# Kernel tuning notes

Measured on AMD Instinct MI355X. Metric: run time of the kernel, lower is better.

Reference implementation:

```python
import jax, jax.numpy as jnp
import numpy as np

H = 16      # num_head
D = 1024    # feat_dim
DK = D // H # per-head dim
B, S = 2, 2048


def setup_inputs() -> dict:
    key = jax.random.key(0)
    ks = jax.random.split(key, 11)
    scale = 1.0 / np.sqrt(D)
    inp = {
        'query': jax.random.normal(ks[0], (B, S, D), jnp.float32),
        'key':   jax.random.normal(ks[1], (B, S, D), jnp.float32),
        'value': jax.random.normal(ks[2], (B, S, D), jnp.float32),
        # causal lower-triangular mask (seq, seq); 0 entries get -1e9
        'mask':  jnp.tril(jnp.ones((S, S), jnp.int32)),
        # torch nn.Linear params: y = x @ W.T + b
        'w_q': jax.random.normal(ks[3], (D, D), jnp.float32) * scale,
        'b_q': jax.random.normal(ks[4], (D,), jnp.float32) * scale,
        'w_k': jax.random.normal(ks[5], (D, D), jnp.float32) * scale,
        'b_k': jax.random.normal(ks[6], (D,), jnp.float32) * scale,
        'w_v': jax.random.normal(ks[7], (D, D), jnp.float32) * scale,
        'b_v': jax.random.normal(ks[8], (D,), jnp.float32) * scale,
        'w_out': jax.random.normal(ks[9], (D, D), jnp.float32) * scale,
        'b_out': jax.random.normal(ks[10], (D,), jnp.float32) * scale,
    }
    return inp


def reference(query, key, value, mask, w_q, b_q, w_k, b_k, w_v, b_v, w_out, b_out):
    b = query.shape[0]
    # projections + split heads -> (b, h, s, d_k)
    def proj(x, w, bias):
        y = x @ w.T + bias
        return y.reshape(b, -1, H, DK).transpose(0, 2, 1, 3)
    q = proj(query, w_q, b_q)
    k = proj(key, w_k, b_k)
    v = proj(value, w_v, b_v)
    # scaled dot-product attention with materialized score matrix
    scores = jnp.einsum('bhqd,bhkd->bhqk', q, k) / np.sqrt(DK).astype(jnp.float32)
    scores = jnp.where(mask == 0, jnp.float32(-1e9), scores)
    attn = jax.nn.softmax(scores, axis=-1)  # dropout is identity in eval mode
    x = jnp.einsum('bhqk,bhkd->bhqd', attn, v)
    x = x.transpose(0, 2, 1, 3).reshape(b, -1, H * DK)
    return x @ w_out.T + b_out
```

## Files before the change

### kernel.cpp

```cpp
#include <hip/hip_runtime.h>

typedef unsigned short u16;
typedef __attribute__((ext_vector_type(8))) short short8;
typedef __attribute__((ext_vector_type(8))) unsigned short u16x8;
typedef __attribute__((ext_vector_type(4))) float floatx4;

#define S2LOG 0.18033688f

__device__ __forceinline__ u16 f2bf(float f) {
    unsigned int u = __float_as_uint(f);
    return (u16)((u + 0x7FFFu + ((u >> 16) & 1u)) >> 16);
}
__device__ __forceinline__ u16 f2bf_hu(float f) {
    return (u16)((__float_as_uint(f) + 0x8000u) >> 16);
}
__device__ __forceinline__ void gl_lds16(const u16* g, u16* l) {
    __builtin_amdgcn_global_load_lds(
        (const __attribute__((address_space(1))) void*)g,
        (__attribute__((address_space(3))) void*)l, 16, 0, 0);
}

__global__ __launch_bounds__(256) void cvt_all(
    const float* __restrict__ q, const float* __restrict__ k, const float* __restrict__ v,
    const float* __restrict__ wq, const float* __restrict__ wk,
    const float* __restrict__ wv, const float* __restrict__ wo,
    u16* __restrict__ ws)
{
    const int b = blockIdx.x, t = threadIdx.x;
    const float* src; u16* dst; long blk;
    if      (b < 2048) { src = q;  dst = ws;            blk = b; }
    else if (b < 4096) { src = k;  dst = ws + 4194304;  blk = b - 2048; }
    else if (b < 6144) { src = v;  dst = ws + 8388608;  blk = b - 4096; }
    else if (b < 6656) { src = wq; dst = ws + 12582912; blk = b - 6144; }
    else if (b < 7168) { src = wk; dst = ws + 13631488; blk = b - 6656; }
    else if (b < 7680) { src = wv; dst = ws + 14680064; blk = b - 7168; }
    else               { src = wo; dst = ws + 15728640; blk = b - 7680; }
    const long i = blk * 2048 + (long)t * 8;
    const float4 a = *(const float4*)(src + i);
    const float4 c = *(const float4*)(src + i + 4);
    u16x8 o;
    o[0] = f2bf(a.x); o[1] = f2bf(a.y); o[2] = f2bf(a.z); o[3] = f2bf(a.w);
    o[4] = f2bf(c.x); o[5] = f2bf(c.y); o[6] = f2bf(c.z); o[7] = f2bf(c.w);
    *(u16x8*)(dst + i) = o;
}

__device__ __forceinline__ void gemm_core64(
    const u16* __restrict__ A, const u16* __restrict__ Bw,
    int m0, int n0, floatx4 (&acc)[2][4])
{
    __shared__ u16 As[2][128 * 64];
    __shared__ u16 Bs[2][64 * 64];
    const int t = threadIdx.x, w = t >> 6;
    const int lane = t & 63, col = lane & 15, quad = lane >> 4;
    const int c7 = col & 7;

#pragma unroll
    for (int i = 0; i < 2; ++i)
#pragma unroll
        for (int j = 0; j < 4; ++j) acc[i][j] = (floatx4)0.f;

    auto stage = [&](int k0, int buf) {
#pragma unroll
        for (int jj = 0; jj < 4; ++jj) {
            const int c = jj * 256 + t;
            const int row = c >> 3, kc = (c & 7) ^ (row & 7);
            gl_lds16(A + (size_t)(m0 + row) * 1024 + k0 + kc * 8,
                     As[buf] + (jj * 256 + w * 64) * 8);
        }
#pragma unroll
        for (int jj = 0; jj < 2; ++jj) {
            const int c = jj * 256 + t;
            const int row = c >> 3, kc = (c & 7) ^ (row & 7);
            gl_lds16(Bw + (size_t)(n0 + row) * 1024 + k0 + kc * 8,
                     Bs[buf] + (jj * 256 + w * 64) * 8);
        }
    };

    stage(0, 0);
    int cur = 0;
    for (int k0 = 0; k0 < 1024; k0 += 64) {
        asm volatile("s_waitcnt vmcnt(0)" ::: "memory");
        __builtin_amdgcn_s_barrier();
        if (k0 + 64 < 1024) stage(k0 + 64, cur ^ 1);
#pragma unroll
        for (int ks = 0; ks < 2; ++ks) {
            const int swz = (ks * 4 + quad) ^ c7;
            short8 af[2], bf[4];
#pragma unroll
            for (int i = 0; i < 2; ++i)
                af[i] = *(const short8*)&As[cur][((w * 32 + i * 16 + col) * 8 + swz) * 8];
#pragma unroll
            for (int j = 0; j < 4; ++j)
                bf[j] = *(const short8*)&Bs[cur][((j * 16 + col) * 8 + swz) * 8];
#pragma unroll
            for (int i = 0; i < 2; ++i)
#pragma unroll
                for (int j = 0; j < 4; ++j)
                    acc[i][j] = __builtin_amdgcn_mfma_f32_16x16x32_bf16(
                        af[i], bf[j], acc[i][j], 0, 0, 0);
        }
        asm volatile("s_waitcnt lgkmcnt(0)" ::: "memory");
        cur ^= 1;
    }
}

__device__ __forceinline__ void gemm_core128(
    const u16* __restrict__ A, const u16* __restrict__ Bw,
    int m0, int n0, floatx4 (&acc)[4][4])
{
    __shared__ u16 As[2][128 * 32];
    __shared__ u16 Bs[2][128 * 32];
    const int t = threadIdx.x, w = t >> 6;
    const int lane = t & 63, col = lane & 15, quad = lane >> 4;
    const int wr = (w >> 1) * 64, wc = (w & 1) * 64;
    const int swz = quad ^ (col & 3) ^ ((col >> 2) & 3);

#pragma unroll
    for (int i = 0; i < 4; ++i)
#pragma unroll
        for (int j = 0; j < 4; ++j) acc[i][j] = (floatx4)0.f;

    auto stage = [&](int k0, int buf) {
#pragma unroll
        for (int jj = 0; jj < 2; ++jj) {
            const int c = jj * 256 + t;
            const int row = c >> 2;
            const int kc = (c & 3) ^ (row & 3) ^ ((row >> 2) & 3);
            gl_lds16(A + (size_t)(m0 + row) * 1024 + k0 + kc * 8,
                     As[buf] + (jj * 256 + w * 64) * 8);
            gl_lds16(Bw + (size_t)(n0 + row) * 1024 + k0 + kc * 8,
                     Bs[buf] + (jj * 256 + w * 64) * 8);
        }
    };

    stage(0, 0);
    int cur = 0;
    for (int k0 = 0; k0 < 1024; k0 += 32) {
        asm volatile("s_waitcnt vmcnt(0)" ::: "memory");
        __builtin_amdgcn_s_barrier();
        if (k0 + 32 < 1024) stage(k0 + 32, cur ^ 1);
        short8 af[4], bf[4];
#pragma unroll
        for (int i = 0; i < 4; ++i)
            af[i] = *(const short8*)&As[cur][((wr + i * 16 + col) * 4 + swz) * 8];
#pragma unroll
        for (int j = 0; j < 4; ++j)
            bf[j] = *(const short8*)&Bs[cur][((wc + j * 16 + col) * 4 + swz) * 8];
        __builtin_amdgcn_s_setprio(1);
#pragma unroll
        for (int i = 0; i < 4; ++i)
#pragma unroll
            for (int j = 0; j < 4; ++j)
                acc[i][j] = __builtin_amdgcn_mfma_f32_16x16x32_bf16(
                    af[i], bf[j], acc[i][j], 0, 0, 0);
        __builtin_amdgcn_s_setprio(0);
        asm volatile("s_waitcnt lgkmcnt(0)" ::: "memory");
        cur ^= 1;
    }
}

__global__ __launch_bounds__(256) void gemm_qkv(
    const u16* __restrict__ xq, const u16* __restrict__ xk, const u16* __restrict__ xv,
    const u16* __restrict__ wqb, const u16* __restrict__ wkb, const u16* __restrict__ wvb,
    const float* __restrict__ bq, const float* __restrict__ bk, const float* __restrict__ bv,
    u16* __restrict__ Qh, u16* __restrict__ Kh, u16* __restrict__ Vt)
{
    const int z = blockIdx.z;
    const u16*   A    = z == 0 ? xq  : z == 1 ? xk  : xv;
    const u16*   Bw   = z == 0 ? wqb : z == 1 ? wkb : wvb;
    const float* bias = z == 0 ? bq  : z == 1 ? bk  : bv;
    u16*         out  = z == 0 ? Qh  : z == 1 ? Kh  : Vt;
    const float  scale = z == 0 ? S2LOG : 1.0f;
    const int m0 = blockIdx.x * 128, n0 = blockIdx.y * 128;

    floatx4 acc[4][4];
    gemm_core128(A, Bw, m0, n0, acc);

    const int t = threadIdx.x, w = t >> 6;
    const int lane = t & 63, col = lane & 15, quad = lane >> 4;
    const int wr = (w >> 1) * 64, wc = (w & 1) * 64;
#pragma unroll
    for (int i = 0; i < 4; ++i)
#pragma unroll
        for (int j = 0; j < 4; ++j)
#pragma unroll
            for (int reg = 0; reg < 4; ++reg) {
                const int gm = m0 + wr + i * 16 + quad * 4 + reg;
                const int gn = n0 + wc + j * 16 + col;
                const float val = (acc[i][j][reg] + bias[gn]) * scale;
                const int bb = gm >> 11, ss = gm & 2047, hh = gn >> 6, dd = gn & 63;
                if (z != 2)
                    out[(((size_t)bb * 16 + hh) * 2048 + ss) * 64 + dd] = f2bf(val);
                else
                    out[(((size_t)bb * 16 + hh) * 64 + dd) * 2048 + ss] = f2bf(val);
            }
}

__global__ __launch_bounds__(256) void gemm_out(
    const u16* __restrict__ A, const u16* __restrict__ Bw,
    const float* __restrict__ bias, float* __restrict__ out)
{
    const int m0 = blockIdx.x * 128, n0 = blockIdx.y * 64;
    floatx4 acc[2][4];
    gemm_core64(A, Bw, m0, n0, acc);
    const int t = threadIdx.x, w = t >> 6;
    const int lane = t & 63, col = lane & 15, quad = lane >> 4;
#pragma unroll
    for (int i = 0; i < 2; ++i)
#pragma unroll
        for (int j = 0; j < 4; ++j)
#pragma unroll
            for (int reg = 0; reg < 4; ++reg) {
                const int gm = m0 + w * 32 + i * 16 + quad * 4 + reg;
                const int gn = n0 + j * 16 + col;
                out[(size_t)gm * 1024 + gn] = acc[i][j][reg] + bias[gn];
            }
}

__global__ __launch_bounds__(256) void attn_mfma(
    const u16* __restrict__ Qh, const u16* __restrict__ Kh,
    const u16* __restrict__ Vt, u16* __restrict__ ctx)
{
    __shared__ u16 QPs[128 * 64];
    __shared__ u16 Ks[2][64 * 64];
    __shared__ u16 Vs[2][64 * 64];
    const int t = threadIdx.x, w = t >> 6;
    const int lane = t & 63, col = lane & 15, quad = lane >> 4;
    const int c7 = col & 7;
    const int bh = blockIdx.y;
    const int qt = (bh < 16) ? (15 - (int)blockIdx.x) : (int)blockIdx.x;
    const int q0 = qt * 128;
    const u16* qg = Qh + ((size_t)bh * 2048 + q0) * 64;
    const u16* kg = Kh + (size_t)bh * 2048 * 64;
    const u16* vg = Vt + (size_t)bh * 2048 * 64;

    auto stage = [&](int tile, int buf) {
#pragma unroll
        for (int jj = 0; jj < 2; ++jj) {
            const int c = jj * 256 + t;
            const int row = c >> 3, kc = (c & 7) ^ (row & 7);
            gl_lds16(kg + (size_t)(tile * 64 + row) * 64 + kc * 8,
                     Ks[buf] + (jj * 256 + w * 64) * 8);
            gl_lds16(vg + (size_t)row * 2048 + tile * 64 + kc * 8,
                     Vs[buf] + (jj * 256 + w * 64) * 8);
        }
    };

#pragma unroll
    for (int jj = 0; jj < 4; ++jj) {
        const int c = jj * 256 + t;
        const int row = c >> 3, kc = (c & 7) ^ (row & 7);
        gl_lds16(qg + (size_t)row * 64 + kc * 8, QPs + (jj * 256 + w * 64) * 8);
    }
    stage(0, 0);
    asm volatile("s_waitcnt vmcnt(4)" ::: "memory");
    __builtin_amdgcn_s_barrier();

    short8 qf[2][2];
#pragma unroll
    for (int i = 0; i < 2; ++i)
#pragma unroll
        for (int ks = 0; ks < 2; ++ks)
            qf[i][ks] = *(const short8*)
                &QPs[((w * 32 + i * 16 + col) * 8 + ((ks * 4 + quad) ^ c7)) * 8];
    asm volatile("s_waitcnt lgkmcnt(0)" ::: "memory");
    __builtin_amdgcn_s_barrier();

    floatx4 oacc[2][4], lacc[2];
#pragma unroll
    for (int i = 0; i < 2; ++i) {
        lacc[i] = (floatx4)0.f;
#pragma unroll
        for (int j = 0; j < 4; ++j) oacc[i][j] = (floatx4)0.f;
    }
    short8 ones;
#pragma unroll
    for (int i = 0; i < 8; ++i) ones[i] = (short)0x3F80;

    const int ktmax = 2 * qt + 1;
    int cur = 0;
    for (int kt = 0; kt <= ktmax; ++kt) {
        asm volatile("s_waitcnt vmcnt(0)" ::: "memory");
        __builtin_amdgcn_s_barrier();
        if (kt + 1 <= ktmax) stage(kt + 1, cur ^ 1);

        floatx4 sa[2][4];
#pragma unroll
        for (int i = 0; i < 2; ++i)
#pragma unroll
            for (int j = 0; j < 4; ++j) sa[i][j] = (floatx4)0.f;
#pragma unroll
        for (int ks = 0; ks < 2; ++ks) {
            const int swz = (ks * 4 + quad) ^ c7;
            short8 kf[4];
#pragma unroll
            for (int jc = 0; jc < 4; ++jc)
                kf[jc] = *(const short8*)&Ks[cur][((jc * 16 + col) * 8 + swz) * 8];
            __builtin_amdgcn_s_setprio(1);
#pragma unroll
            for (int i = 0; i < 2; ++i)
#pragma unroll
                for (int jc = 0; jc < 4; ++jc)
                    sa[i][jc] = __builtin_amdgcn_mfma_f32_16x16x32_bf16(
                        qf[i][ks], kf[jc], sa[i][jc], 0, 0, 0);
            __builtin_amdgcn_s_setprio(0);
        }
        const bool pm = (kt >= 2 * qt);
#pragma unroll
        for (int i = 0; i < 2; ++i)
#pragma unroll
            for (int reg = 0; reg < 4; ++reg) {
                const int prow = w * 32 + i * 16 + quad * 4 + reg;
                const int qrow = q0 + prow;
                const int pr7 = (quad * 4 + reg) & 7;
                u16* pr = &QPs[prow * 64 + (col & 7)];
#pragma unroll
                for (int jc = 0; jc < 4; ++jc) {
                    float p = __builtin_amdgcn_exp2f(sa[i][jc][reg]);
                    if (pm && (kt * 64 + jc * 16 + col > qrow)) p = 0.f;
                    pr[((2 * jc + (col >> 3)) ^ pr7) << 3] = f2bf_hu(p);
                }
            }
#pragma unroll
        for (int ks = 0; ks < 2; ++ks) {
            const int swz = (ks * 4 + quad) ^ c7;
            short8 pf[2], vf[4];
#pragma unroll
            for (int i = 0; i < 2; ++i)
                pf[i] = *(const short8*)
                    &QPs[((w * 32 + i * 16 + col) * 8 + swz) * 8];
#pragma unroll
            for (int jd = 0; jd < 4; ++jd)
                vf[jd] = *(const short8*)&Vs[cur][((jd * 16 + col) * 8 + swz) * 8];
            __builtin_amdgcn_s_setprio(1);
#pragma unroll
            for (int i = 0; i < 2; ++i) {
                lacc[i] = __builtin_amdgcn_mfma_f32_16x16x32_bf16(pf[i], ones, lacc[i], 0, 0, 0);
#pragma unroll
                for (int jd = 0; jd < 4; ++jd)
                    oacc[i][jd] = __builtin_amdgcn_mfma_f32_16x16x32_bf16(
                        pf[i], vf[jd], oacc[i][jd], 0, 0, 0);
            }
            __builtin_amdgcn_s_setprio(0);
        }
        cur ^= 1;
    }

    const int bb = bh >> 4, hh = bh & 15;
#pragma unroll
    for (int i = 0; i < 2; ++i)
#pragma unroll
        for (int reg = 0; reg < 4; ++reg) {
            const float inv = __builtin_amdgcn_rcpf(lacc[i][reg]);
            const int qrow = q0 + w * 32 + i * 16 + quad * 4 + reg;
#pragma unroll
            for (int jd = 0; jd < 4; ++jd)
                ctx[((size_t)bb * 2048 + qrow) * 1024 + hh * 64 + jd * 16 + col] =
                    f2bf(oacc[i][jd][reg] * inv);
        }
}

extern "C" void kernel_launch(void* const* d_in, const int* in_sizes, int n_in,
                              void* d_out, int out_size, void* d_ws, size_t ws_size,
                              hipStream_t stream)
{
    const float* query = (const float*)d_in[0];
    const float* key   = (const float*)d_in[1];
    const float* value = (const float*)d_in[2];
    const float* w_q   = (const float*)d_in[4];
    const float* b_q   = (const float*)d_in[5];
    const float* w_k   = (const float*)d_in[6];
    const float* b_k   = (const float*)d_in[7];
    const float* w_v   = (const float*)d_in[8];
    const float* b_v   = (const float*)d_in[9];
    const float* w_out = (const float*)d_in[10];
    const float* b_out = (const float*)d_in[11];

    u16* W = (u16*)d_ws;
    u16* xq  = W;
    u16* xk  = W + 4194304;
    u16* xv  = W + 8388608;
    u16* wqb = W + 12582912;
    u16* wkb = W + 13631488;
    u16* wvb = W + 14680064;
    u16* wob = W + 15728640;
    u16* Qh  = W + 16777216;
    u16* Kh  = W + 20971520;
    u16* Vtw = W + 25165824;
    u16* ctx = W + 29360128;

    hipLaunchKernelGGL(cvt_all, dim3(8192), dim3(256), 0, stream,
                       query, key, value, w_q, w_k, w_v, w_out, W);

    hipLaunchKernelGGL(gemm_qkv, dim3(32, 8, 3), dim3(256), 0, stream,
                       xq, xk, xv, wqb, wkb, wvb, b_q, b_k, b_v, Qh, Kh, Vtw);

    hipLaunchKernelGGL(attn_mfma, dim3(16, 32), dim3(256), 0, stream, Qh, Kh, Vtw, ctx);

    hipLaunchKernelGGL(gemm_out, dim3(32, 16), dim3(256), 0, stream,
                       ctx, wob, b_out, (float*)d_out);
}
```

Baseline: 239.3 us.

## Switch attention to 32x32x16 MFMA with register-resident P via permlane swap

Rewrites the attention inner loop to use 32x32x16 bf16 MFMA, computing S transposed (K times Q) so the exponentiated probabilities can be rearranged in registers with v_permlane32_swap instead of being written to and re-read from LDS. The row-sum is kept as a per-lane scalar accumulator and combined by shuffles at the end, replacing the extra ones-MFMA. The aim is to cut LDS round-trips and MFMA instruction count. The trade-offs are different register pressure, the removal of s_setprio hints, and reliance on a correct lane mapping for the transposed layout.

```diff
diff --git a/kernel.cpp b/kernel.cpp
--- a/kernel.cpp
+++ b/kernel.cpp
@@ -4,6 +4,7 @@
 typedef __attribute__((ext_vector_type(8))) short short8;
 typedef __attribute__((ext_vector_type(8))) unsigned short u16x8;
 typedef __attribute__((ext_vector_type(4))) float floatx4;
+typedef __attribute__((ext_vector_type(16))) float floatx16;
 
 #define S2LOG 0.18033688f
 
@@ -225,8 +226,10 @@
     __shared__ u16 Ks[2][64 * 64];
     __shared__ u16 Vs[2][64 * 64];
     const int t = threadIdx.x, w = t >> 6;
-    const int lane = t & 63, col = lane & 15, quad = lane >> 4;
-    const int c7 = col & 7;
+    const int lane = t & 63;
+    const int col = lane & 31;
+    const int hi  = lane >> 5;
+    const int l7  = lane & 7;
     const int bh = blockIdx.y;
     const int qt = (bh < 16) ? (15 - (int)blockIdx.x) : (int)blockIdx.x;
     const int q0 = qt * 128;
@@ -256,26 +259,16 @@
     asm volatile("s_waitcnt vmcnt(4)" ::: "memory");
     __builtin_amdgcn_s_barrier();
 
-    short8 qf[2][2];
-#pragma unroll
-    for (int i = 0; i < 2; ++i)
-#pragma unroll
-        for (int ks = 0; ks < 2; ++ks)
-            qf[i][ks] = *(const short8*)
-                &QPs[((w * 32 + i * 16 + col) * 8 + ((ks * 4 + quad) ^ c7)) * 8];
-    asm volatile("s_waitcnt lgkmcnt(0)" ::: "memory");
-    __builtin_amdgcn_s_barrier();
-
-    floatx4 oacc[2][4], lacc[2];
-#pragma unroll
-    for (int i = 0; i < 2; ++i) {
-        lacc[i] = (floatx4)0.f;
-#pragma unroll
-        for (int j = 0; j < 4; ++j) oacc[i][j] = (floatx4)0.f;
-    }
-    short8 ones;
-#pragma unroll
-    for (int i = 0; i < 8; ++i) ones[i] = (short)0x3F80;
+    short8 qf[4];
+#pragma unroll
+    for (int tq = 0; tq < 4; ++tq)
+        qf[tq] = *(const short8*)
+            &QPs[((w * 32 + col) * 8 + ((2 * tq + hi) ^ l7)) * 8];
+
+    floatx16 oacc[2];
+    oacc[0] = (floatx16)0.f; oacc[1] = (floatx16)0.f;
+    float ls = 0.f;
+    const int qrow = q0 + w * 32 + col;
 
     const int ktmax = 2 * qt + 1;
     int cur = 0;
@@ -283,81 +276,77 @@
         asm volatile("s_waitcnt vmcnt(0)" ::: "memory");
         __builtin_amdgcn_s_barrier();
         if (kt + 1 <= ktmax) stage(kt + 1, cur ^ 1);
-
-        floatx4 sa[2][4];
-#pragma unroll
-        for (int i = 0; i < 2; ++i)
-#pragma unroll
-            for (int j = 0; j < 4; ++j) sa[i][j] = (floatx4)0.f;
-#pragma unroll
-        for (int ks = 0; ks < 2; ++ks) {
-            const int swz = (ks * 4 + quad) ^ c7;
+        const bool pm = (kt >= 2 * qt);
+
+#pragma unroll
+        for (int sub = 0; sub < 2; ++sub) {
+            const int krow = sub * 32 + col;
             short8 kf[4];
 #pragma unroll
-            for (int jc = 0; jc < 4; ++jc)
-                kf[jc] = *(const short8*)&Ks[cur][((jc * 16 + col) * 8 + swz) * 8];
-            __builtin_amdgcn_s_setprio(1);
-#pragma unroll
-            for (int i = 0; i < 2; ++i)
-#pragma unroll
-                for (int jc = 0; jc < 4; ++jc)
-                    sa[i][jc] = __builtin_amdgcn_mfma_f32_16x16x32_bf16(
-                        qf[i][ks], kf[jc], sa[i][jc], 0, 0, 0);
-            __builtin_amdgcn_s_setprio(0);
-        }
-        const bool pm = (kt >= 2 * qt);
-#pragma unroll
-        for (int i = 0; i < 2; ++i)
-#pragma unroll
-            for (int reg = 0; reg < 4; ++reg) {
-                const int prow = w * 32 + i * 16 + quad * 4 + reg;
-                const int qrow = q0 + prow;
-                const int pr7 = (quad * 4 + reg) & 7;
-                u16* pr = &QPs[prow * 64 + (col & 7)];
-#pragma unroll
-                for (int jc = 0; jc < 4; ++jc) {
-                    float p = __builtin_amdgcn_exp2f(sa[i][jc][reg]);
-                    if (pm && (kt * 64 + jc * 16 + col > qrow)) p = 0.f;
-                    pr[((2 * jc + (col >> 3)) ^ pr7) << 3] = f2bf_hu(p);
+            for (int tq = 0; tq < 4; ++tq)
+                kf[tq] = *(const short8*)
+                    &Ks[cur][(krow * 8 + ((2 * tq + hi) ^ l7)) * 8];
+
+            floatx16 sacc = (floatx16)0.f;
+#pragma unroll
+            for (int tq = 0; tq < 4; ++tq)
+                sacc = __builtin_amdgcn_mfma_f32_32x32x16_bf16(
+                    kf[tq], qf[tq], sacc, 0, 0, 0);
+
+            u16 ph[16];
+#pragma unroll
+            for (int r = 0; r < 16; ++r) {
+                float pe = __builtin_amdgcn_exp2f(sacc[r]);
+                u16 h = f2bf_hu(pe);
+                if (pm && (kt * 64 + sub * 32 + (r & 3) + 8 * (r >> 2) + 4 * hi > qrow))
+                    h = 0;
+                ph[r] = h;
+                ls += __uint_as_float((unsigned)h << 16);
+            }
+
+            short8 pa[2];
+#pragma unroll
+            for (int s = 0; s < 2; ++s) {
+                unsigned A0 = (unsigned)ph[8 * s + 0] | ((unsigned)ph[8 * s + 1] << 16);
+                unsigned A1 = (unsigned)ph[8 * s + 2] | ((unsigned)ph[8 * s + 3] << 16);
+                unsigned B0 = (unsigned)ph[8 * s + 4] | ((unsigned)ph[8 * s + 5] << 16);
+                unsigned B1 = (unsigned)ph[8 * s + 6] | ((unsigned)ph[8 * s + 7] << 16);
+                asm("v_permlane32_swap_b32 %0, %1" : "+v"(A0), "+v"(B0));
+                asm("v_permlane32_swap_b32 %0, %1" : "+v"(A1), "+v"(B1));
+                union { unsigned u[4]; short8 s8; } cv;
+                cv.u[0] = A0; cv.u[1] = A1; cv.u[2] = B0; cv.u[3] = B1;
+                pa[s] = cv.s8;
+            }
+
+#pragma unroll
+            for (int dt = 0; dt < 2; ++dt) {
+                const int vrow = dt * 32 + col;
+#pragma unroll
+                for (int s = 0; s < 2; ++s) {
+                    const int ksv = sub * 2 + s;
+                    short8 vf = *(const short8*)
+                        &Vs[cur][(vrow * 8 + ((2 * ksv + hi) ^ l7)) * 8];
+                    oacc[dt] = __builtin_amdgcn_mfma_f32_32x32x16_bf16(
+                        pa[s], vf, oacc[dt], 0, 0, 0);
                 }
             }
-#pragma unroll
-        for (int ks = 0; ks < 2; ++ks) {
-            const int swz = (ks * 4 + quad) ^ c7;
-            short8 pf[2], vf[4];
-#pragma unroll
-            for (int i = 0; i < 2; ++i)
-                pf[i] = *(const short8*)
-                    &QPs[((w * 32 + i * 16 + col) * 8 + swz) * 8];
-#pragma unroll
-            for (int jd = 0; jd < 4; ++jd)
-                vf[jd] = *(const short8*)&Vs[cur][((jd * 16 + col) * 8 + swz) * 8];
-            __builtin_amdgcn_s_setprio(1);
-#pragma unroll
-            for (int i = 0; i < 2; ++i) {
-                lacc[i] = __builtin_amdgcn_mfma_f32_16x16x32_bf16(pf[i], ones, lacc[i], 0, 0, 0);
-#pragma unroll
-                for (int jd = 0; jd < 4; ++jd)
-                    oacc[i][jd] = __builtin_amdgcn_mfma_f32_16x16x32_bf16(
-                        pf[i], vf[jd], oacc[i][jd], 0, 0, 0);
-            }
-            __builtin_amdgcn_s_setprio(0);
         }
         cur ^= 1;
     }
 
+    const float lt = ls + __shfl_xor(ls, 32);
     const int bb = bh >> 4, hh = bh & 15;
 #pragma unroll
-    for (int i = 0; i < 2; ++i)
-#pragma unroll
-        for (int reg = 0; reg < 4; ++reg) {
-            const float inv = __builtin_amdgcn_rcpf(lacc[i][reg]);
-            const int qrow = q0 + w * 32 + i * 16 + quad * 4 + reg;
-#pragma unroll
-            for (int jd = 0; jd < 4; ++jd)
-                ctx[((size_t)bb * 2048 + qrow) * 1024 + hh * 64 + jd * 16 + col] =
-                    f2bf(oacc[i][jd][reg] * inv);
-        }
+    for (int reg = 0; reg < 16; ++reg) {
+        const int qr = (reg & 3) + 8 * (reg >> 2) + 4 * hi;
+        const float lq = __shfl(lt, qr, 64);
+        const float inv = __builtin_amdgcn_rcpf(lq);
+        const int qrs = q0 + w * 32 + qr;
+#pragma unroll
+        for (int dt = 0; dt < 2; ++dt)
+            ctx[((size_t)bb * 2048 + qrs) * 1024 + hh * 64 + dt * 32 + col] =
+                f2bf(oacc[dt][reg] * inv);
+    }
 }
 
 extern "C" void kernel_launch(void* const* d_in, const int* in_sizes, int n_in,
```

After: 242.3 us. Within noise of the previous version (+1.3%).
